# Performance work log

Measured on AMD Instinct MI355X. Metric: run time of the kernel, lower is better.

Reference implementation:

```python
import jax, jax.numpy as jnp
import numpy as np

B, S, D, HD, P = 4, 8192, 1024, 128, 32
EPS_LN = 1e-5

def setup_inputs() -> dict:
    key = jax.random.key(0)
    ks = jax.random.split(key, 12)
    x      = jax.random.normal(ks[0], (B, S, D), dtype=jnp.float32)
    W_proj = jax.random.normal(ks[1], (8, D, HD), dtype=jnp.float32) * 0.02
    freqs  = jax.random.normal(ks[2], (8, HD), dtype=jnp.float32) * 0.01
    W_pol  = jax.random.normal(ks[3], (8, HD, P), dtype=jnp.float32) * 0.05
    b_pol  = jnp.zeros((8, P), jnp.float32)
    W_imp1 = jax.random.normal(ks[4], (1, 16), dtype=jnp.float32) * 0.5
    b_imp1 = jnp.zeros((16,), jnp.float32)
    W_imp2 = jax.random.normal(ks[5], (16, 1), dtype=jnp.float32) * 0.5
    b_imp2 = jnp.zeros((1,), jnp.float32)
    W_out  = jax.random.normal(ks[6], (D, D), dtype=jnp.float32) * 0.02
    b_out  = jnp.zeros((D,), jnp.float32)
    gamma  = jnp.ones((D,), jnp.float32)
    beta   = jnp.zeros((D,), jnp.float32)
    return dict(x=x, W_proj=W_proj, freqs=freqs, W_pol=W_pol, b_pol=b_pol,
                W_imp1=W_imp1, b_imp1=b_imp1, W_imp2=W_imp2, b_imp2=b_imp2,
                W_out=W_out, b_out=b_out, gamma=gamma, beta=beta)

def reference(x, W_proj, freqs, W_pol, b_pol, W_imp1, b_imp1, W_imp2, b_imp2,
              W_out, b_out, gamma, beta):
    # heads[i] = (x @ W_proj[i]) * cos(pi * freqs[i])   -> (8, B, S, HD)
    heads = jnp.einsum('bsd,hde->hbse', x, W_proj) * jnp.cos(freqs * jnp.pi)[:, None, None, :]

    # --- GuaXiangDuiChong: impedance matrix (B, 8, 8) ---
    hm = heads.mean(axis=2)                                   # (8, B, HD)
    pv = jnp.tanh(jnp.einsum('hbd,hdp->bhp', hm, W_pol) + b_pol[None])  # (B, 8, P)
    pm = pv / jnp.maximum(jnp.linalg.norm(pv, axis=-1, keepdims=True), 1e-12)
    dp = jnp.einsum('bhp,bgp->bhg', pm, pm)                   # (B, 8, 8)
    z = jax.nn.gelu(dp[..., None] * W_imp1[0] + b_imp1, approximate=False)  # (B,8,8,16)
    imp = jax.nn.softplus(jnp.einsum('bhgk,ko->bhgo', z, W_imp2)[..., 0] + b_imp2[0])
    imp = imp * (1.0 - jnp.eye(8, dtype=imp.dtype))           # zero diagonal

    # --- head mixing. Causal masked-mean collapses to row scale (s+1)/S ---
    coeff = (0.1 / (1.0 + imp)) * (1.0 - jnp.eye(8, dtype=imp.dtype))  # (B,8,8), j!=i
    mix = jnp.einsum('big,gbsd->ibsd', coeff, heads)          # (8, B, S, HD)
    causal_scale = (jnp.arange(S, dtype=x.dtype) + 1.0) / S   # (S,)
    out_heads = heads + causal_scale[None, None, :, None] * mix

    merged = out_heads.transpose(1, 2, 0, 3).reshape(B, S, D)
    proj = jnp.einsum('bsd,de->bse', merged, W_out) + b_out   # dropout = identity (eval)
    y = proj + x
    mu = y.mean(axis=-1, keepdims=True)
    var = y.var(axis=-1, keepdims=True)
    y = (y - mu) * jax.lax.rsqrt(var + EPS_LN) * gamma + beta
    return y, imp
```

## Files before the change

kernel.cpp:

```cpp
#include <hip/hip_runtime.h>
#include <hip/hip_bf16.h>
#include <math.h>

typedef __bf16 bf16;
typedef __bf16 bf16x2 __attribute__((ext_vector_type(2)));
typedef __bf16 bf16x4 __attribute__((ext_vector_type(4)));
typedef __bf16 bf16x8 __attribute__((ext_vector_type(8)));
typedef float  f32x4  __attribute__((ext_vector_type(4)));

#define NB 4
#define SS 8192
#define DD 1024
#define MM 32768
#define KK 1024
#define NN 1024
#define PI_F 3.14159265358979323846f

__device__ __forceinline__ void gl2lds16(const bf16* g, bf16* l) {
    __builtin_amdgcn_global_load_lds(
        (const __attribute__((address_space(1))) void*)g,
        (__attribute__((address_space(3))) void*)l, 16, 0, 0);
}

__global__ __launch_bounds__(256) void prep_all(const float* __restrict__ x,
                                                bf16* __restrict__ xb,
                                                const float* __restrict__ W_proj,
                                                const float* __restrict__ freqs,
                                                const float* __restrict__ W_out,
                                                bf16* __restrict__ WbT1,
                                                bf16* __restrict__ WoT,
                                                float* __restrict__ hm) {
    int blk = blockIdx.x;
    if (blk < MM) {
        size_t i = (size_t)blk * 1024 + threadIdx.x * 4;
        float4 v = *(const float4*)&x[i];
        bf16x4 o;
        o[0] = (bf16)v.x; o[1] = (bf16)v.y; o[2] = (bf16)v.z; o[3] = (bf16)v.w;
        *(bf16x4*)&xb[i] = o;
    } else {
        int idx = (blk - MM) * 256 + threadIdx.x;
        int n = idx >> 10, k = idx & 1023;
        int h = n >> 7, d = n & 127;
        float c = cosf(PI_F * freqs[n]);
        WbT1[idx] = (bf16)(W_proj[(size_t)h * (DD * 128) + (size_t)k * 128 + d] * c);
        WoT[idx]  = (bf16)(W_out[(size_t)k * DD + n]);
        if (idx < NB * DD) hm[idx] = 0.0f;
    }
}


#define FENCE  asm volatile("" ::: "memory")
#define BARRIER do { FENCE; __builtin_amdgcn_s_barrier(); FENCE; } while (0)
#define PRIO1  __builtin_amdgcn_s_setprio(1)
#define PRIO0  __builtin_amdgcn_s_setprio(0)
#define VMC(N) asm volatile("s_waitcnt vmcnt(" #N ")" ::: "memory")
#define NOPS   ((void)0)

#define STG(g0, g1, uk, ldsBase)                                  \
    gl2lds16((g0) + (uk), &sm[(ldsBase) + w * 512]);              \
    gl2lds16((g1) + (uk), &sm[(ldsBase) + 4096 + w * 512]);

#define READ_A2(MQ, ab)                                                          \
    _Pragma("unroll") for (int m_ = 0; m_ < 4; ++m_) {                           \
        a[m_ * 2 + 0] = *(const bf16x8*)&sm[(ab) + aoff0 + ((MQ)*64 + m_*16)*64];\
        a[m_ * 2 + 1] = *(const bf16x8*)&sm[(ab) + aoff1 + ((MQ)*64 + m_*16)*64];\
    }
#define READ_B2(NQ, bfr, bb)                                                     \
    _Pragma("unroll") for (int n_ = 0; n_ < 2; ++n_) {                           \
        bfr[n_ * 2 + 0] = *(const bf16x8*)&sm[(bb) + boff0 + ((NQ)*32 + n_*16)*64];\
        bfr[n_ * 2 + 1] = *(const bf16x8*)&sm[(bb) + boff1 + ((NQ)*32 + n_*16)*64];\
    }

#define MFMA_Q(MQ, NQ, bfr)                                                    \
    _Pragma("unroll") for (int m_ = 0; m_ < 4; ++m_)                           \
    _Pragma("unroll") for (int n_ = 0; n_ < 2; ++n_)                           \
    _Pragma("unroll") for (int ks_ = 0; ks_ < 2; ++ks_)                        \
        acc[(MQ) * 4 + m_][(NQ) * 2 + n_] =                                    \
            __builtin_amdgcn_mfma_f32_16x16x32_bf16(                           \
                a[m_ * 2 + ks_], bfr[n_ * 2 + ks_],                            \
                acc[(MQ) * 4 + m_][(NQ) * 2 + n_], 0, 0, 0);

#define ITER(uk1, STG3, STG4, STG5, STG6, STG7, STG8, VM4, VM8)                \
  {                                                                    \
    BARRIER; STG(gA00, gA01, (uk1), 16384);                                    \
    PRIO1; READ_A2(0, 0); READ_B2(0, blo, 32768);                              \
    MFMA_Q(0, 0, blo); PRIO0;                                                  \
                                                                       \
    BARRIER; STG(gA10, gA11, (uk1), 24576);                                    \
    PRIO1; READ_B2(1, bhi, 32768); MFMA_Q(0, 1, bhi); PRIO0;                   \
                                                                       \
    BARRIER; STG3;                                                             \
    PRIO1; READ_A2(1, 0); MFMA_Q(1, 1, bhi); PRIO0;                            \
                                                     \
    BARRIER; STG4; VM4;                                                        \
    PRIO1; MFMA_Q(1, 0, blo); PRIO0;                                           \
                                                                       \
    BARRIER; STG5;                                                             \
    PRIO1; READ_A2(0, 16384); READ_B2(0, blo, 49152);                          \
    MFMA_Q(0, 0, blo); PRIO0;                                                  \
                                                                       \
    BARRIER; STG6;                                                             \
    PRIO1; READ_B2(1, bhi, 49152); MFMA_Q(0, 1, bhi); PRIO0;                   \
                                                                       \
    BARRIER; STG7;                                                             \
    PRIO1; READ_A2(1, 16384); MFMA_Q(1, 1, bhi); PRIO0;                        \
                                                     \
    BARRIER; STG8; VM8;                                                        \
    PRIO1; MFMA_Q(1, 0, blo); PRIO0;                                           \
  }

template <int MODE>
__global__ __launch_bounds__(512, 2)
void gemm256(const bf16* __restrict__ A, int lda, const bf16* __restrict__ Bt,
             bf16* __restrict__ Cstr, const bf16* __restrict__ residb,
             const float* __restrict__ bias, float* __restrict__ hm) {
    __shared__ bf16 sm[65536];
    const int tid = threadIdx.x;
    const int lane = tid & 63, w = tid >> 6;
    const int wr = w >> 2, wc = w & 3;
    const int l15 = lane & 15, l4 = lane >> 4;

    int wg = blockIdx.x;
    int swz = (wg & 7) * 64 + (wg >> 3);
    const int mt = swz >> 2, ntile = swz & 3;
    const int row0 = mt * 256, col0 = ntile * 256;

    const int aoff0 = (wr * 128 + l15) * 64 + ((l4 ^ (l15 & 7)) << 3);
    const int aoff1 = aoff0 ^ 32;
    const int boff0 = (wc * 64 + l15) * 64 + ((l4 ^ (l15 & 7)) << 3);
    const int boff1 = boff0 ^ 32;

    const int srow = tid >> 3;
    const int scb  = (tid & 7) ^ (srow & 7);
    const bf16* gA00 = A + (size_t)(row0 + srow) * lda + scb * 8;
    const bf16* gA01 = gA00 + (size_t)64 * lda;
    const bf16* gA10 = gA00 + (size_t)128 * lda;
    const bf16* gA11 = gA00 + (size_t)192 * lda;
    const bf16* gB00 = Bt + (size_t)(col0 + srow) * 1024 + scb * 8;
    const bf16* gB01 = gB00 + 64 * 1024;
    const bf16* gB10 = gB00 + 128 * 1024;
    const bf16* gB11 = gB00 + 192 * 1024;

    f32x4 acc[8][4] = {};
    bf16x8 a[8], blo[4], bhi[4];

    STG(gA00, gA01, 0,  0);     STG(gA10, gA11, 0,  8192);
    STG(gB00, gB01, 0,  32768); STG(gB10, gB11, 0,  40960);
    STG(gA00, gA01, 64, 16384); STG(gA10, gA11, 64, 24576);
    STG(gB00, gB01, 64, 49152); STG(gB10, gB11, 64, 57344);
    VMC(0);

#pragma unroll 1
    for (int i = 0; i < 7; ++i) {
        const int uk1 = (2 * i + 1) * 64;
        const int uk2 = (2 * i + 2) * 64;
        const int uk3 = (2 * i + 3) * 64;
        ITER(uk1,
             STG(gB00, gB01, uk2, 32768), STG(gB10, gB11, uk2, 40960),
             STG(gA00, gA01, uk2, 0),     STG(gA10, gA11, uk2, 8192),
             STG(gB00, gB01, uk3, 49152), STG(gB10, gB11, uk3, 57344),
             VMC(4), VMC(4));
    }
    ITER(960, NOPS, NOPS, NOPS, NOPS, NOPS, NOPS, VMC(0), NOPS);

    if (MODE == 0) {
        const int batch = row0 >> 13;
#pragma unroll
        for (int mg = 0; mg < 8; ++mg) {
            int rbase = row0 + wr * 128 + (mg >> 2) * 64 + (mg & 3) * 16 + l4 * 4;
#pragma unroll
            for (int j = 0; j < 4; ++j) {
                size_t row = rbase + j;
#pragma unroll
                for (int ng = 0; ng < 4; ++ng) {
                    int col = col0 + wc * 64 + ng * 16 + l15;
                    Cstr[row * 2048 + col] = (bf16)acc[mg][ng][j];
                }
            }
        }
#pragma unroll
        for (int ng = 0; ng < 4; ++ng) {
            float s = 0;
#pragma unroll
            for (int mg = 0; mg < 8; ++mg)
#pragma unroll
                for (int j = 0; j < 4; ++j) s += acc[mg][ng][j];
            int col = col0 + wc * 64 + ng * 16 + l15;
            atomicAdd(&hm[batch * DD + col], s);
        }
    } else {
        float bi[4];
#pragma unroll
        for (int ng = 0; ng < 4; ++ng) bi[ng] = bias[col0 + wc * 64 + ng * 16 + l15];
#pragma unroll
        for (int mg = 0; mg < 8; ++mg) {
            int rbase = row0 + wr * 128 + (mg >> 2) * 64 + (mg & 3) * 16 + l4 * 4;
#pragma unroll
            for (int j = 0; j < 4; ++j) {
                size_t row = rbase + j;
#pragma unroll
                for (int ng = 0; ng < 4; ++ng) {
                    int col = col0 + wc * 64 + ng * 16 + l15;
                    Cstr[row * 2048 + col] =
                        (bf16)(acc[mg][ng][j] + bi[ng] + (float)residb[row * 1024 + col]);
                }
            }
        }
    }
}

__global__ __launch_bounds__(1024) void imp_k(const float* __restrict__ hm,
                                              const float* __restrict__ W_pol,
                                              const float* __restrict__ b_pol,
                                              const float* __restrict__ W_imp1,
                                              const float* __restrict__ b_imp1,
                                              const float* __restrict__ W_imp2,
                                              const float* __restrict__ b_imp2,
                                              float* __restrict__ imp_out,
                                              float* __restrict__ coeff) {
    __shared__ float pm_s[32][32];
    int tid = threadIdx.x;
    int bh = tid >> 5, p = tid & 31;
    int b = bh >> 3, h = bh & 7;
    float a = b_pol[h * 32 + p];
    for (int d = 0; d < 128; ++d)
        a += hm[b * DD + h * 128 + d] * (1.0f / SS) * W_pol[(h * 128 + d) * 32 + p];
    float pv = tanhf(a);
    pm_s[bh][p] = pv;
    __syncthreads();
    float ss = 0;
    for (int q = 0; q < 32; ++q) ss += pm_s[bh][q] * pm_s[bh][q];
    float pmv = pv / fmaxf(sqrtf(ss), 1e-12f);
    __syncthreads();
    pm_s[bh][p] = pmv;
    __syncthreads();
    if (tid < 256) {
        int b2 = tid >> 6, h2 = (tid >> 3) & 7, g = tid & 7;
        float dp = 0;
        for (int q = 0; q < 32; ++q) dp += pm_s[b2 * 8 + h2][q] * pm_s[b2 * 8 + g][q];
        float a2 = 0;
        for (int kk = 0; kk < 16; ++kk) {
            float zin = dp * W_imp1[kk] + b_imp1[kk];
            float zg = 0.5f * zin * (1.0f + erff(zin * 0.70710678118654752f));
            a2 += zg * W_imp2[kk];
        }
        float spin = a2 + b_imp2[0];
        float impv = (spin > 20.0f) ? spin : log1pf(expf(spin));
        if (h2 == g) impv = 0.0f;
        imp_out[tid] = impv;
        coeff[tid] = (h2 == g) ? 0.0f : 0.1f / (1.0f + impv);
    }
}

__global__ __launch_bounds__(256) void mix_k(const char* __restrict__ slots,
                                             const float* __restrict__ coeff,
                                             char* __restrict__ slots_w) {
    __shared__ float cf[64];
    int tid = threadIdx.x;
    size_t r0 = (size_t)blockIdx.x * 4;
    int b = (int)(r0 >> 13);
    if (tid < 64) cf[tid] = coeff[b * 64 + tid];
    __syncthreads();
    int lr = tid >> 6;
    int d2 = tid & 63;
    size_t r = r0 + lr;
    int s = (int)(r & (SS - 1));
    float cs = (float)(s + 1) * (1.0f / SS);
    const bf16* hrow = (const bf16*)(slots + r * 4096);
    bf16* mrow = (bf16*)(slots_w + r * 4096 + 2048);
    float v0[8], v1[8];
#pragma unroll
    for (int g = 0; g < 8; ++g) {
        bf16x2 v = *(const bf16x2*)&hrow[g * 128 + d2 * 2];
        v0[g] = (float)v[0]; v1[g] = (float)v[1];
    }
#pragma unroll
    for (int h = 0; h < 8; ++h) {
        float a0 = 0, a1 = 0;
#pragma unroll
        for (int g = 0; g < 8; ++g) {
            float c = cf[h * 8 + g];
            a0 += c * v0[g]; a1 += c * v1[g];
        }
        bf16x2 o;
        o[0] = (bf16)(v0[h] + cs * a0);
        o[1] = (bf16)(v1[h] + cs * a1);
        *(bf16x2*)&mrow[h * 128 + d2 * 2] = o;
    }
}

__global__ __launch_bounds__(256) void ln_k(char* __restrict__ slots,
                                            const float* __restrict__ gamma,
                                            const float* __restrict__ beta) {
    size_t r = blockIdx.x;
    int tid = threadIdx.x;
    const bf16* zrow = (const bf16*)(slots + r * 4096);
    float* yrow = (float*)(slots + r * 4096);
    int e0 = tid * 4;
    bf16x4 zv = *(const bf16x4*)&zrow[e0];
    float vx = (float)zv[0], vy = (float)zv[1], vz = (float)zv[2], vw = (float)zv[3];
    float sum = vx + vy + vz + vw;
    float sq  = vx * vx + vy * vy + vz * vz + vw * vw;
    for (int off = 32; off > 0; off >>= 1) {
        sum += __shfl_down(sum, off);
        sq  += __shfl_down(sq, off);
    }
    __shared__ float red[8];
    int lane = tid & 63, wv = tid >> 6;
    if (lane == 0) { red[wv] = sum; red[4 + wv] = sq; }
    __syncthreads();
    float tot = red[0] + red[1] + red[2] + red[3];
    float tsq = red[4] + red[5] + red[6] + red[7];
    float mu  = tot * (1.0f / DD);
    float var = tsq * (1.0f / DD) - mu * mu;
    float rs  = rsqrtf(var + 1e-5f);
    float4 g4 = *(const float4*)&gamma[e0];
    float4 b4 = *(const float4*)&beta[e0];
    float4 o;
    o.x = (vx - mu) * rs * g4.x + b4.x;
    o.y = (vy - mu) * rs * g4.y + b4.y;
    o.z = (vz - mu) * rs * g4.z + b4.z;
    o.w = (vw - mu) * rs * g4.w + b4.w;
    *(float4*)&yrow[e0] = o;
}

extern "C" void kernel_launch(void* const* d_in, const int* in_sizes, int n_in,
                              void* d_out, int out_size, void* d_ws, size_t ws_size,
                              hipStream_t stream) {
    const float* x      = (const float*)d_in[0];
    const float* W_proj = (const float*)d_in[1];
    const float* freqs  = (const float*)d_in[2];
    const float* W_pol  = (const float*)d_in[3];
    const float* b_pol  = (const float*)d_in[4];
    const float* W_imp1 = (const float*)d_in[5];
    const float* b_imp1 = (const float*)d_in[6];
    const float* W_imp2 = (const float*)d_in[7];
    const float* b_imp2 = (const float*)d_in[8];
    const float* W_out  = (const float*)d_in[9];
    const float* b_out  = (const float*)d_in[10];
    const float* gamma  = (const float*)d_in[11];
    const float* beta   = (const float*)d_in[12];

    char* ws = (char*)d_ws;
    bf16* xb     = (bf16*)ws;
    bf16* WbT1   = (bf16*)(ws + ((size_t)64 << 20));
    bf16* WoT    = (bf16*)(ws + ((size_t)66 << 20));
    float* hm    = (float*)(ws + ((size_t)68 << 20));
    float* coeff = (float*)(ws + ((size_t)68 << 20) + 16384);

    char* slots = (char*)d_out;
    float* imp_out = (float*)d_out + (size_t)MM * DD;

    prep_all<<<MM + 4096, 256, 0, stream>>>(x, xb, W_proj, freqs, W_out,
                                            WbT1, WoT, hm);

    gemm256<0><<<512, 512, 0, stream>>>(xb, 1024, WbT1, (bf16*)slots,
                                        nullptr, nullptr, hm);

    imp_k<<<1, 1024, 0, stream>>>(hm, W_pol, b_pol, W_imp1, b_imp1, W_imp2, b_imp2,
                                  imp_out, coeff);

    mix_k<<<MM / 4, 256, 0, stream>>>(slots, coeff, slots);

    gemm256<1><<<512, 512, 0, stream>>>((const bf16*)slots + 1024, 2048, WoT,
                                        (bf16*)slots, xb, b_out, nullptr);

    ln_k<<<MM, 256, 0, stream>>>(slots, gamma, beta);
}
```

Measured before the change: 266.1 us.

## Fuse fp32-to-bf16 conversion of x into first GEMM's A-tile loading

Removes the separate pass that converted x to bf16. The first GEMM now loads fp32 x tiles into registers, converts them, and writes swizzled bf16 to LDS, with a reworked pipeline schedule and extra lgkmcnt waits. The second GEMM reads the fp32 residual x directly instead of the bf16 copy. This saves a full read and write of the 128MB activation but raises register pressure and adds VALU conversion plus synchronous LDS stores in the GEMM's inner loop.

```diff
diff --git a/kernel.cpp b/kernel.cpp
--- a/kernel.cpp
+++ b/kernel.cpp
@@ -22,38 +22,27 @@
         (__attribute__((address_space(3))) void*)l, 16, 0, 0);
 }
 
-__global__ __launch_bounds__(256) void prep_all(const float* __restrict__ x,
-                                                bf16* __restrict__ xb,
-                                                const float* __restrict__ W_proj,
-                                                const float* __restrict__ freqs,
-                                                const float* __restrict__ W_out,
-                                                bf16* __restrict__ WbT1,
-                                                bf16* __restrict__ WoT,
-                                                float* __restrict__ hm) {
-    int blk = blockIdx.x;
-    if (blk < MM) {
-        size_t i = (size_t)blk * 1024 + threadIdx.x * 4;
-        float4 v = *(const float4*)&x[i];
-        bf16x4 o;
-        o[0] = (bf16)v.x; o[1] = (bf16)v.y; o[2] = (bf16)v.z; o[3] = (bf16)v.w;
-        *(bf16x4*)&xb[i] = o;
-    } else {
-        int idx = (blk - MM) * 256 + threadIdx.x;
-        int n = idx >> 10, k = idx & 1023;
-        int h = n >> 7, d = n & 127;
-        float c = cosf(PI_F * freqs[n]);
-        WbT1[idx] = (bf16)(W_proj[(size_t)h * (DD * 128) + (size_t)k * 128 + d] * c);
-        WoT[idx]  = (bf16)(W_out[(size_t)k * DD + n]);
-        if (idx < NB * DD) hm[idx] = 0.0f;
-    }
-}
-
+__global__ __launch_bounds__(256) void prep_w(const float* __restrict__ W_proj,
+                                              const float* __restrict__ freqs,
+                                              const float* __restrict__ W_out,
+                                              bf16* __restrict__ WbT1,
+                                              bf16* __restrict__ WoT,
+                                              float* __restrict__ hm) {
+    int idx = blockIdx.x * 256 + threadIdx.x;
+    int n = idx >> 10, k = idx & 1023;
+    int h = n >> 7, d = n & 127;
+    float c = cosf(PI_F * freqs[n]);
+    WbT1[idx] = (bf16)(W_proj[(size_t)h * (DD * 128) + (size_t)k * 128 + d] * c);
+    WoT[idx]  = (bf16)(W_out[(size_t)k * DD + n]);
+    if (idx < NB * DD) hm[idx] = 0.0f;
+}
 
 #define FENCE  asm volatile("" ::: "memory")
 #define BARRIER do { FENCE; __builtin_amdgcn_s_barrier(); FENCE; } while (0)
 #define PRIO1  __builtin_amdgcn_s_setprio(1)
 #define PRIO0  __builtin_amdgcn_s_setprio(0)
 #define VMC(N) asm volatile("s_waitcnt vmcnt(" #N ")" ::: "memory")
+#define LGKM0  asm volatile("s_waitcnt lgkmcnt(0)" ::: "memory")
 #define NOPS   ((void)0)
 
 #define STG(g0, g1, uk, ldsBase)                                  \
@@ -80,40 +69,45 @@
                 a[m_ * 2 + ks_], bfr[n_ * 2 + ks_],                            \
                 acc[(MQ) * 4 + m_][(NQ) * 2 + n_], 0, 0, 0);
 
-#define ITER(uk1, STG3, STG4, STG5, STG6, STG7, STG8, VM4, VM8)                \
-  {                                                                    \
-    BARRIER; STG(gA00, gA01, (uk1), 16384);                                    \
-    PRIO1; READ_A2(0, 0); READ_B2(0, blo, 32768);                              \
-    MFMA_Q(0, 0, blo); PRIO0;                                                  \
-                                                                       \
-    BARRIER; STG(gA10, gA11, (uk1), 24576);                                    \
+#define ISSA(uk)                                                               \
+    areg[0] = *(const f32x4*)(gAh0c0 + (uk)); areg[1] = *(const f32x4*)(gAh0c0 + (uk) + 4); \
+    areg[2] = *(const f32x4*)(gAh0c1 + (uk)); areg[3] = *(const f32x4*)(gAh0c1 + (uk) + 4); \
+    areg[4] = *(const f32x4*)(gAh1c0 + (uk)); areg[5] = *(const f32x4*)(gAh1c0 + (uk) + 4); \
+    areg[6] = *(const f32x4*)(gAh1c1 + (uk)); areg[7] = *(const f32x4*)(gAh1c1 + (uk) + 4);
+
+#define CVT1(dst, lo, hi)                                                      \
+    { bf16x8 w_; w_[0]=(bf16)(lo).x; w_[1]=(bf16)(lo).y; w_[2]=(bf16)(lo).z;   \
+      w_[3]=(bf16)(lo).w; w_[4]=(bf16)(hi).x; w_[5]=(bf16)(hi).y;              \
+      w_[6]=(bf16)(hi).z; w_[7]=(bf16)(hi).w; *(bf16x8*)(dst) = w_; }
+
+#define WRA(ab)                                                                \
+    CVT1(&sm[(ab) + wAoff0],        areg[0], areg[1]);                         \
+    CVT1(&sm[(ab) + wAoff1],        areg[2], areg[3]);                         \
+    CVT1(&sm[(ab) + 8192 + wAoff0], areg[4], areg[5]);                         \
+    CVT1(&sm[(ab) + 8192 + wAoff1], areg[6], areg[7]);
+
+#define ITER1(uk1, uk2, ISS2, STG3, STG4, STG7, STG8, VM3, VM7, WR7)           \
+  { BARRIER; ISSA(uk1);                                                        \
+    PRIO1; READ_A2(0, 0); READ_B2(0, blo, 32768); MFMA_Q(0, 0, blo); PRIO0;    \
+    BARRIER;                                                                   \
     PRIO1; READ_B2(1, bhi, 32768); MFMA_Q(0, 1, bhi); PRIO0;                   \
-                                                                       \
-    BARRIER; STG3;                                                             \
+    BARRIER; STG3; VM3; WRA(16384);                                            \
     PRIO1; READ_A2(1, 0); MFMA_Q(1, 1, bhi); PRIO0;                            \
-                                                     \
-    BARRIER; STG4; VM4;                                                        \
-    PRIO1; MFMA_Q(1, 0, blo); PRIO0;                                           \
-                                                                       \
-    BARRIER; STG5;                                                             \
-    PRIO1; READ_A2(0, 16384); READ_B2(0, blo, 49152);                          \
-    MFMA_Q(0, 0, blo); PRIO0;                                                  \
-                                                                       \
-    BARRIER; STG6;                                                             \
+    BARRIER; STG4;                                                             \
+    PRIO1; MFMA_Q(1, 0, blo); PRIO0; LGKM0;                                    \
+    BARRIER; ISS2;                                                             \
+    PRIO1; READ_A2(0, 16384); READ_B2(0, blo, 49152); MFMA_Q(0, 0, blo); PRIO0;\
+    BARRIER;                                                                   \
     PRIO1; READ_B2(1, bhi, 49152); MFMA_Q(0, 1, bhi); PRIO0;                   \
-                                                                       \
-    BARRIER; STG7;                                                             \
+    BARRIER; STG7; VM7; WR7;                                                   \
     PRIO1; READ_A2(1, 16384); MFMA_Q(1, 1, bhi); PRIO0;                        \
-                                                     \
-    BARRIER; STG8; VM8;                                                        \
-    PRIO1; MFMA_Q(1, 0, blo); PRIO0;                                           \
+    BARRIER; STG8;                                                             \
+    PRIO1; MFMA_Q(1, 0, blo); PRIO0; LGKM0;                                    \
   }
 
-template <int MODE>
 __global__ __launch_bounds__(512, 2)
-void gemm256(const bf16* __restrict__ A, int lda, const bf16* __restrict__ Bt,
-             bf16* __restrict__ Cstr, const bf16* __restrict__ residb,
-             const float* __restrict__ bias, float* __restrict__ hm) {
+void gemm_g1(const float* __restrict__ X, const bf16* __restrict__ Bt,
+             bf16* __restrict__ Cstr, float* __restrict__ hm) {
     __shared__ bf16 sm[65536];
     const int tid = threadIdx.x;
     const int lane = tid & 63, w = tid >> 6;
@@ -130,8 +124,115 @@
     const int boff0 = (wc * 64 + l15) * 64 + ((l4 ^ (l15 & 7)) << 3);
     const int boff1 = boff0 ^ 32;
 
+    const int rA = tid >> 2;
+    const int c0 = (tid & 3) * 2;
+    const int lg0 = c0 ^ (rA & 7), lg1 = (c0 + 1) ^ (rA & 7);
+    const float* gAh0c0 = X + (size_t)(row0 + rA) * 1024 + lg0 * 8;
+    const float* gAh0c1 = X + (size_t)(row0 + rA) * 1024 + lg1 * 8;
+    const float* gAh1c0 = gAh0c0 + (size_t)128 * 1024;
+    const float* gAh1c1 = gAh0c1 + (size_t)128 * 1024;
+    const int wAoff0 = rA * 64 + c0 * 8;
+    const int wAoff1 = wAoff0 + 8;
+
     const int srow = tid >> 3;
     const int scb  = (tid & 7) ^ (srow & 7);
+    const bf16* gB00 = Bt + (size_t)(col0 + srow) * 1024 + scb * 8;
+    const bf16* gB01 = gB00 + 64 * 1024;
+    const bf16* gB10 = gB00 + 128 * 1024;
+    const bf16* gB11 = gB00 + 192 * 1024;
+
+    f32x4 acc[8][4] = {};
+    bf16x8 a[8], blo[4], bhi[4];
+    f32x4 areg[8];
+
+    ISSA(0);
+    STG(gB00, gB01, 0,  32768); STG(gB10, gB11, 0,  40960);
+    STG(gB00, gB01, 64, 49152); STG(gB10, gB11, 64, 57344);
+    VMC(8);
+    WRA(0);
+    VMC(4);
+    LGKM0;
+
+#pragma unroll 1
+    for (int i = 0; i < 7; ++i) {
+        const int uk1 = (2 * i + 1) * 64;
+        const int uk2 = (2 * i + 2) * 64;
+        const int uk3 = (2 * i + 3) * 64;
+        ITER1(uk1, uk2, ISSA(uk2),
+              STG(gB00, gB01, uk2, 32768), STG(gB10, gB11, uk2, 40960),
+              STG(gB00, gB01, uk3, 49152), STG(gB10, gB11, uk3, 57344),
+              VMC(2), VMC(2), WRA(0));
+    }
+    ITER1(960, 0, NOPS, NOPS, NOPS, NOPS, NOPS, VMC(0), VMC(0), NOPS);
+
+    const int batch = row0 >> 13;
+#pragma unroll
+    for (int mg = 0; mg < 8; ++mg) {
+        int rbase = row0 + wr * 128 + (mg >> 2) * 64 + (mg & 3) * 16 + l4 * 4;
+#pragma unroll
+        for (int j = 0; j < 4; ++j) {
+            size_t row = rbase + j;
+#pragma unroll
+            for (int ng = 0; ng < 4; ++ng) {
+                int col = col0 + wc * 64 + ng * 16 + l15;
+                Cstr[row * 2048 + col] = (bf16)acc[mg][ng][j];
+            }
+        }
+    }
+#pragma unroll
+    for (int ng = 0; ng < 4; ++ng) {
+        float s = 0;
+#pragma unroll
+        for (int mg = 0; mg < 8; ++mg)
+#pragma unroll
+            for (int j = 0; j < 4; ++j) s += acc[mg][ng][j];
+        int col = col0 + wc * 64 + ng * 16 + l15;
+        atomicAdd(&hm[batch * DD + col], s);
+    }
+}
+
+#define ITER2(uk1, STG3, STG4, STG5, STG6, STG7, STG8, VM4, VM8)               \
+  { BARRIER; STG(gA00, gA01, (uk1), 16384);                                    \
+    PRIO1; READ_A2(0, 0); READ_B2(0, blo, 32768); MFMA_Q(0, 0, blo); PRIO0;    \
+    BARRIER; STG(gA10, gA11, (uk1), 24576);                                    \
+    PRIO1; READ_B2(1, bhi, 32768); MFMA_Q(0, 1, bhi); PRIO0;                   \
+    BARRIER; STG3;                                                             \
+    PRIO1; READ_A2(1, 0); MFMA_Q(1, 1, bhi); PRIO0;                            \
+    BARRIER; STG4; VM4;                                                        \
+    PRIO1; MFMA_Q(1, 0, blo); PRIO0;                                           \
+    BARRIER; STG5;                                                             \
+    PRIO1; READ_A2(0, 16384); READ_B2(0, blo, 49152); MFMA_Q(0, 0, blo); PRIO0;\
+    BARRIER; STG6;                                                             \
+    PRIO1; READ_B2(1, bhi, 49152); MFMA_Q(0, 1, bhi); PRIO0;                   \
+    BARRIER; STG7;                                                             \
+    PRIO1; READ_A2(1, 16384); MFMA_Q(1, 1, bhi); PRIO0;                        \
+    BARRIER; STG8; VM8;                                                        \
+    PRIO1; MFMA_Q(1, 0, blo); PRIO0;                                           \
+  }
+
+__global__ __launch_bounds__(512, 2)
+void gemm_g2(const bf16* __restrict__ A, const bf16* __restrict__ Bt,
+             bf16* __restrict__ Cstr, const float* __restrict__ resid,
+             const float* __restrict__ bias) {
+    __shared__ bf16 sm[65536];
+    const int tid = threadIdx.x;
+    const int lane = tid & 63, w = tid >> 6;
+    const int wr = w >> 2, wc = w & 3;
+    const int l15 = lane & 15, l4 = lane >> 4;
+
+    int wg = blockIdx.x;
+    int swz = (wg & 7) * 64 + (wg >> 3);
+    const int mt = swz >> 2, ntile = swz & 3;
+    const int row0 = mt * 256, col0 = ntile * 256;
+
+    const int aoff0 = (wr * 128 + l15) * 64 + ((l4 ^ (l15 & 7)) << 3);
+    const int aoff1 = aoff0 ^ 32;
+    const int boff0 = (wc * 64 + l15) * 64 + ((l4 ^ (l15 & 7)) << 3);
+    const int boff1 = boff0 ^ 32;
+
+    const int srow = tid >> 3;
+    const int scb  = (tid & 7) ^ (srow & 7);
+    const int lda = 2048;
     const bf16* gA00 = A + (size_t)(row0 + srow) * lda + scb * 8;
     const bf16* gA01 = gA00 + (size_t)64 * lda;
     const bf16* gA10 = gA00 + (size_t)128 * lda;
@@ -155,55 +256,28 @@
         const int uk1 = (2 * i + 1) * 64;
         const int uk2 = (2 * i + 2) * 64;
         const int uk3 = (2 * i + 3) * 64;
-        ITER(uk1,
-             STG(gB00, gB01, uk2, 32768), STG(gB10, gB11, uk2, 40960),
-             STG(gA00, gA01, uk2, 0),     STG(gA10, gA11, uk2, 8192),
-             STG(gB00, gB01, uk3, 49152), STG(gB10, gB11, uk3, 57344),
-             VMC(4), VMC(4));
-    }
-    ITER(960, NOPS, NOPS, NOPS, NOPS, NOPS, NOPS, VMC(0), NOPS);
-
-    if (MODE == 0) {
-        const int batch = row0 >> 13;
-#pragma unroll
-        for (int mg = 0; mg < 8; ++mg) {
-            int rbase = row0 + wr * 128 + (mg >> 2) * 64 + (mg & 3) * 16 + l4 * 4;
-#pragma unroll
-            for (int j = 0; j < 4; ++j) {
-                size_t row = rbase + j;
-#pragma unroll
-                for (int ng = 0; ng < 4; ++ng) {
-                    int col = col0 + wc * 64 + ng * 16 + l15;
-                    Cstr[row * 2048 + col] = (bf16)acc[mg][ng][j];
-                }
-            }
-        }
-#pragma unroll
-        for (int ng = 0; ng < 4; ++ng) {
-            float s = 0;
-#pragma unroll
-            for (int mg = 0; mg < 8; ++mg)
-#pragma unroll
-                for (int j = 0; j < 4; ++j) s += acc[mg][ng][j];
-            int col = col0 + wc * 64 + ng * 16 + l15;
-            atomicAdd(&hm[batch * DD + col], s);
-        }
-    } else {
-        float bi[4];
-#pragma unroll
-        for (int ng = 0; ng < 4; ++ng) bi[ng] = bias[col0 + wc * 64 + ng * 16 + l15];
-#pragma unroll
-        for (int mg = 0; mg < 8; ++mg) {
-            int rbase = row0 + wr * 128 + (mg >> 2) * 64 + (mg & 3) * 16 + l4 * 4;
-#pragma unroll
-            for (int j = 0; j < 4; ++j) {
-                size_t row = rbase + j;
-#pragma unroll
-                for (int ng = 0; ng < 4; ++ng) {
-                    int col = col0 + wc * 64 + ng * 16 + l15;
-                    Cstr[row * 2048 + col] =
-                        (bf16)(acc[mg][ng][j] + bi[ng] + (float)residb[row * 1024 + col]);
-                }
+        ITER2(uk1,
+              STG(gB00, gB01, uk2, 32768), STG(gB10, gB11, uk2, 40960),
+              STG(gA00, gA01, uk2, 0),     STG(gA10, gA11, uk2, 8192),
+              STG(gB00, gB01, uk3, 49152), STG(gB10, gB11, uk3, 57344),
+              VMC(4), VMC(4));
+    }
+    ITER2(960, NOPS, NOPS, NOPS, NOPS, NOPS, NOPS, VMC(0), NOPS);
+
+    float bi[4];
+#pragma unroll
+    for (int ng = 0; ng < 4; ++ng) bi[ng] = bias[col0 + wc * 64 + ng * 16 + l15];
+#pragma unroll
+    for (int mg = 0; mg < 8; ++mg) {
+        int rbase = row0 + wr * 128 + (mg >> 2) * 64 + (mg & 3) * 16 + l4 * 4;
+#pragma unroll
+        for (int j = 0; j < 4; ++j) {
+            size_t row = rbase + j;
+#pragma unroll
+            for (int ng = 0; ng < 4; ++ng) {
+                int col = col0 + wc * 64 + ng * 16 + l15;
+                Cstr[row * 2048 + col] =
+                    (bf16)(acc[mg][ng][j] + bi[ng] + resid[row * 1024 + col]);
             }
         }
     }
@@ -342,28 +416,25 @@
     const float* beta   = (const float*)d_in[12];
 
     char* ws = (char*)d_ws;
-    bf16* xb     = (bf16*)ws;
-    bf16* WbT1   = (bf16*)(ws + ((size_t)64 << 20));
-    bf16* WoT    = (bf16*)(ws + ((size_t)66 << 20));
-    float* hm    = (float*)(ws + ((size_t)68 << 20));
-    float* coeff = (float*)(ws + ((size_t)68 << 20) + 16384);
+    bf16* WbT1   = (bf16*)ws;
+    bf16* WoT    = (bf16*)(ws + ((size_t)2 << 20));
+    float* hm    = (float*)(ws + ((size_t)4 << 20));
+    float* coeff = (float*)(ws + ((size_t)4 << 20) + 16384);
 
     char* slots = (char*)d_out;
     float* imp_out = (float*)d_out + (size_t)MM * DD;
 
-    prep_all<<<MM + 4096, 256, 0, stream>>>(x, xb, W_proj, freqs, W_out,
-                                            WbT1, WoT, hm);
-
-    gemm256<0><<<512, 512, 0, stream>>>(xb, 1024, WbT1, (bf16*)slots,
-                                        nullptr, nullptr, hm);
+    prep_w<<<4096, 256, 0, stream>>>(W_proj, freqs, W_out, WbT1, WoT, hm);
+
+    gemm_g1<<<512, 512, 0, stream>>>(x, WbT1, (bf16*)slots, hm);
 
     imp_k<<<1, 1024, 0, stream>>>(hm, W_pol, b_pol, W_imp1, b_imp1, W_imp2, b_imp2,
                                   imp_out, coeff);
 
     mix_k<<<MM / 4, 256, 0, stream>>>(slots, coeff, slots);
 
-    gemm256<1><<<512, 512, 0, stream>>>((const bf16*)slots + 1024, 2048, WoT,
-                                        (bf16*)slots, xb, b_out, nullptr);
+    gemm_g2<<<512, 512, 0, stream>>>((const bf16*)slots + 1024, WoT,
+                                     (bf16*)slots, x, b_out);
 
     ln_k<<<MM, 256, 0, stream>>>(slots, gamma, beta);
 }
```

Result: slower. 302.3 us (+13.6%).
